# Performance work log

Measured on AMD Instinct MI355X. Metric: run time of the kernel, lower is better.

Reference implementation:

```python
import jax, jax.numpy as jnp
import numpy as np

N_NODES = 100000
N_EDGES = 1600000
K = 3  # TAGConv default hops


def _make_lin(key, out_dim, in_dim):
    # K+1 bias-free linears (stacked) + one shared output bias, per PyG TAGConv
    kw, = jax.random.split(key, 1)
    scale = 1.0 / np.sqrt(in_dim)
    W = jax.random.uniform(kw, (K + 1, out_dim, in_dim), jnp.float32, -scale, scale)
    b = jnp.zeros((out_dim,), jnp.float32)
    return W, b


def setup_inputs() -> dict:
    key = jax.random.key(0)
    ks = jax.random.split(key, 6)
    x = jax.random.normal(ks[0], (N_NODES, 128), jnp.float32)
    edge_index = jax.random.randint(ks[1], (2, N_EDGES), 0, N_NODES, jnp.int64)
    W1, b1 = _make_lin(ks[2], 128, 128)
    W2, b2 = _make_lin(ks[3], 64, 128)
    W3, b3 = _make_lin(ks[4], 16, 64)
    return {"x": x, "edge_index": edge_index, "W1": W1, "b1": b1,
            "W2": W2, "b2": b2, "W3": W3, "b3": b3}


def _tagconv(x, row, col, norm, W, b, n):
    # out = sum_k lin_k(A_norm^k x) + b ; message x_j*norm gathered at col
    out = jnp.einsum('nd,od->no', x, W[0])
    h = x
    for k in range(1, W.shape[0]):
        h = jax.ops.segment_sum(norm[:, None] * h[row], col, num_segments=n)
        out = out + jnp.einsum('nd,od->no', h, W[k])
    return out + b


def _dropout(x, key, p=0.5):
    keep = jax.random.bernoulli(key, 1.0 - p, x.shape)
    return jnp.where(keep, x / (1.0 - p), 0.0)


def reference(x, edge_index, W1, b1, W2, b2, W3, b3):
    n = x.shape[0]
    row, col = edge_index[0], edge_index[1]
    # gcn_norm without self-loops (TAGConv default)
    deg = jax.ops.segment_sum(jnp.ones(row.shape[0], x.dtype), col, num_segments=n)
    dis = jnp.where(deg > 0, 1.0 / jnp.sqrt(jnp.where(deg > 0, deg, 1.0)), 0.0)
    norm = dis[row] * dis[col]

    dk1, dk2 = jax.random.split(jax.random.key(42))
    h = _tagconv(x, row, col, norm, W1, b1, n)
    h = _dropout(h, dk1)
    h = _tagconv(h, row, col, norm, W2, b2, n)
    h = jax.nn.elu(h)
    h = _dropout(h, dk2)
    h = _tagconv(h, row, col, norm, W3, b3, n)
    return h
```

## Files before the change

kernel.cpp:

```cpp
#include <hip/hip_runtime.h>
#include <stdint.h>
#include <math.h>

#define N_NODES 100000
#define N_EDGES 1600000

typedef __bf16 bf16_t;
typedef __attribute__((ext_vector_type(4))) __bf16 bf16x4;
typedef __attribute__((ext_vector_type(8))) __bf16 bf16x8;
typedef __attribute__((ext_vector_type(4))) float f32x4;

__device__ __forceinline__ f32x4 mfma16(bf16x8 a, bf16x8 b, f32x4 c) {
  return __builtin_amdgcn_mfma_f32_16x16x32_bf16(a, b, c, 0, 0, 0);
}

__device__ __host__ __forceinline__ uint32_t rotl32(uint32_t v, int d) {
  return (v << d) | (v >> (32 - d));
}

__device__ __host__ __forceinline__ void threefry2x32(uint32_t k0, uint32_t k1,
                                                      uint32_t x0, uint32_t x1,
                                                      uint32_t& o0, uint32_t& o1) {
  uint32_t ks0 = k0, ks1 = k1, ks2 = k0 ^ k1 ^ 0x1BD11BDAu;
  x0 += ks0; x1 += ks1;
#define TF_R(r) { x0 += x1; x1 = rotl32(x1, r); x1 ^= x0; }
  TF_R(13) TF_R(15) TF_R(26) TF_R(6)
  x0 += ks1; x1 += ks2 + 1u;
  TF_R(17) TF_R(29) TF_R(16) TF_R(24)
  x0 += ks2; x1 += ks0 + 2u;
  TF_R(13) TF_R(15) TF_R(26) TF_R(6)
  x0 += ks0; x1 += ks1 + 3u;
  TF_R(17) TF_R(29) TF_R(16) TF_R(24)
  x0 += ks1; x1 += ks2 + 4u;
  TF_R(13) TF_R(15) TF_R(26) TF_R(6)
  x0 += ks2; x1 += ks0 + 5u;
#undef TF_R
  o0 = x0; o1 = x1;
}

__device__ __forceinline__ float drop_scale(uint32_t idx, uint32_t k0, uint32_t k1) {
  uint32_t o0, o1;
  threefry2x32(k0, k1, 0u, idx, o0, o1);
  uint32_t bits = o0 ^ o1;
  float u = __uint_as_float((bits >> 9) | 0x3f800000u) - 1.0f;
  return (u < 0.5f) ? 2.0f : 0.0f;
}

__global__ __launch_bounds__(256) void detect_kernel(const int* __restrict__ ei,
                                                     int* __restrict__ found_nonzero) {
  int idx = blockIdx.x * 256 + threadIdx.x;
  size_t j = (size_t)idx * 781;
  if (ei[2 * j + 1] != 0) atomicOr(found_nonzero, 1);
}

__device__ __forceinline__ int edge_row(const int* ei, bool i32, int e) {
  return i32 ? ei[e] : ei[2 * (size_t)e];
}
__device__ __forceinline__ int edge_col(const int* ei, bool i32, int e) {
  return i32 ? ei[N_EDGES + e] : ei[2 * ((size_t)N_EDGES + (size_t)e)];
}

#define BKT_SHIFT 8
#define NBKT 391
#define BKT_CAP 6144
#define EPB 8192
#define NBLK 196
#define SCAN_M (NBKT * NBLK)

__global__ __launch_bounds__(256) void hist_kernel(const int* __restrict__ ei,
                                                   const int* __restrict__ flag,
                                                   int* __restrict__ hist) {
  __shared__ int h[NBKT];
  const int t = threadIdx.x, blk = blockIdx.x;
  for (int i = t; i < NBKT; i += 256) h[i] = 0;
  __syncthreads();
  const bool i32 = *flag != 0;
  const int e0 = blk * EPB;
  for (int i = t; i < EPB; i += 256) {
    int e = e0 + i;
    if (e < N_EDGES) atomicAdd(&h[edge_col(ei, i32, e) >> BKT_SHIFT], 1);
  }
  __syncthreads();
  for (int i = t; i < NBKT; i += 256) hist[i * NBLK + blk] = h[i];
}

__global__ __launch_bounds__(1024) void binscan_kernel(const int* __restrict__ hist,
                                                       int* __restrict__ S) {
  __shared__ int sh[1024];
  const int t = threadIdx.x;
  const int CH = (SCAN_M + 1023) / 1024;
  int lo = t * CH, hi = min(lo + CH, SCAN_M);
  int s = 0;
  for (int i = lo; i < hi; ++i) s += hist[i];
  sh[t] = s;
  __syncthreads();
  for (int ofs = 1; ofs < 1024; ofs <<= 1) {
    int u = (t >= ofs) ? sh[t - ofs] : 0;
    __syncthreads();
    sh[t] += u;
    __syncthreads();
  }
  int p = sh[t] - s;
  for (int i = lo; i < hi; ++i) { S[i] = p; p += hist[i]; }
  if (t == 1023) S[SCAN_M] = p;
}

__global__ __launch_bounds__(256) void binfill_kernel(const int* __restrict__ ei,
                                                      const int* __restrict__ flag,
                                                      const int* __restrict__ S,
                                                      int2* __restrict__ bins) {
  __shared__ int cur[NBKT];
  const int t = threadIdx.x, blk = blockIdx.x;
  for (int i = t; i < NBKT; i += 256) cur[i] = S[i * NBLK + blk];
  __syncthreads();
  const bool i32 = *flag != 0;
  const int e0 = blk * EPB;
  for (int i = t; i < EPB; i += 256) {
    int e = e0 + i;
    if (e < N_EDGES) {
      int r = edge_row(ei, i32, e);
      int c = edge_col(ei, i32, e);
      int p = atomicAdd(&cur[c >> BKT_SHIFT], 1);
      bins[p] = make_int2(r, c);
    }
  }
}

__global__ __launch_bounds__(512) void degdis_kernel(const int2* __restrict__ bins,
                                                     const int* __restrict__ S,
                                                     float* __restrict__ dis,
                                                     int* __restrict__ rptr) {
  __shared__ int h[256];
  __shared__ int sc[256];
  const int b = blockIdx.x, t = threadIdx.x;
  const int Bb = S[b * NBLK];
  const int Be = S[(b + 1) * NBLK];
  if (t < 256) h[t] = 0;
  __syncthreads();
  for (int i = t; i < Be - Bb; i += 512)
    atomicAdd(&h[bins[Bb + i].y & 255], 1);
  __syncthreads();
  if (t < 256) sc[t] = h[t];
  __syncthreads();
  for (int ofs = 1; ofs < 256; ofs <<= 1) {
    int u = 0;
    if (t >= ofs && t < 256) u = sc[t - ofs];
    __syncthreads();
    if (t < 256) sc[t] += u;
    __syncthreads();
  }
  const int c0 = b << BKT_SHIFT;
  if (t < 256 && c0 + t < N_NODES) {
    int d = h[t];
    dis[c0 + t] = (d > 0) ? (1.0f / sqrtf((float)d)) : 0.0f;
    rptr[c0 + t] = Bb + sc[t] - d;
  }
  if (b == NBKT - 1 && t == 0) rptr[N_NODES] = N_EDGES;
}

__global__ __launch_bounds__(512) void scatter_kernel(
    const int2* __restrict__ bins, const float* __restrict__ dis,
    const int* __restrict__ rptr, int2* __restrict__ erec) {
  __shared__ int loff[256];
  __shared__ int lcur[256];
  __shared__ float ldis[256];
  __shared__ int2 stage[BKT_CAP];
  const int b = blockIdx.x;
  const int c0 = b << BKT_SHIFT;
  const int nn = min(256, N_NODES - c0);
  const int t = threadIdx.x;
  const int base = rptr[c0];
  if (t < nn) {
    loff[t] = rptr[c0 + t] - base;
    lcur[t] = 0;
    ldis[t] = dis[c0 + t];
  }
  __syncthreads();
  const int cnt = min(rptr[c0 + nn] - base, BKT_CAP);
  for (int i = t; i < cnt; i += 512) {
    int2 rec = bins[base + i];
    int lc = rec.y & 255;
    float nrm = dis[rec.x] * ldis[lc];
    int p = atomicAdd(&lcur[lc], 1);
    stage[loff[lc] + p] = make_int2(rec.x, __float_as_int(nrm));
  }
  __syncthreads();
  for (int i = t; i < cnt; i += 512) erec[base + i] = stage[i];
}

__global__ __launch_bounds__(256) void wcvt_kernel(
    const float* __restrict__ W1, const float* __restrict__ W2,
    const float* __restrict__ W3,
    bf16_t* __restrict__ Wb1, bf16_t* __restrict__ Wb2,
    bf16_t* __restrict__ Wb3) {
  int i = blockIdx.x * 256 + threadIdx.x;
  if (i < 65536) Wb1[i] = (bf16_t)W1[i];
  if (i < 32768) Wb2[i] = (bf16_t)W2[i];
  if (i < 4096)  Wb3[i] = (bf16_t)W3[i];
}

template <int DIN, int LOG_DOUT, int NCH, bool YB, bool AHL>
__global__ __launch_bounds__(256) void matmul_mfma_kernel(
    const void* __restrict__ hA, const void* __restrict__ hAlo,
    const bf16_t* __restrict__ Wb, const float* __restrict__ bias,
    float* __restrict__ y0, void* __restrict__ y1,
    void* __restrict__ y2, void* __restrict__ y3) {
  constexpr int LDK = DIN + 8;
  constexpr int DOUT = 1 << LOG_DOUT;
  constexpr int KI = DIN / 32;
  __shared__ bf16_t sm[2][64 * LDK];
  const int m0 = blockIdx.x * 64;
  const int tid = threadIdx.x;

  if (AHL) {
    constexpr int NL = 64 * DIN / 8 / 256;
#pragma unroll
    for (int it = 0; it < NL; ++it) {
      int idx = tid + it * 256;
      int r = idx / (DIN / 8), cc = (idx % (DIN / 8)) * 8;
      int gm = m0 + r;
      uint4 vh = make_uint4(0, 0, 0, 0), vl = make_uint4(0, 0, 0, 0);
      if (gm < N_NODES) {
        vh = ((const uint4*)hA)[((size_t)gm * DIN + cc) >> 3];
        vl = ((const uint4*)hAlo)[((size_t)gm * DIN + cc) >> 3];
      }
      *(uint4*)&sm[0][r * LDK + cc] = vh;
      *(uint4*)&sm[1][r * LDK + cc] = vl;
    }
  } else {
    constexpr int NL = 64 * DIN / 4 / 256;
    union U4 { bf16_t b[4]; uint2 u; };
#pragma unroll
    for (int it = 0; it < NL; ++it) {
      int idx = tid + it * 256;
      int r = idx / (DIN / 4), cc = (idx % (DIN / 4)) * 4;
      int gm = m0 + r;
      float4 v = (gm < N_NODES) ? ((const float4*)hA)[((size_t)gm * DIN + cc) >> 2]
                                : make_float4(0.f, 0.f, 0.f, 0.f);
      U4 hi, lo;
      hi.b[0] = (bf16_t)v.x; lo.b[0] = (bf16_t)(v.x - (float)hi.b[0]);
      hi.b[1] = (bf16_t)v.y; lo.b[1] = (bf16_t)(v.y - (float)hi.b[1]);
      hi.b[2] = (bf16_t)v.z; lo.b[2] = (bf16_t)(v.z - (float)hi.b[2]);
      hi.b[3] = (bf16_t)v.w; lo.b[3] = (bf16_t)(v.w - (float)hi.b[3]);
      *(uint2*)&sm[0][r * LDK + cc] = hi.u;
      *(uint2*)&sm[1][r * LDK + cc] = lo.u;
    }
  }
  __syncthreads();

  const int w = tid >> 6, lane = tid & 63;
  const int wm = w & 1, wn = w >> 1;
  const int quad = lane >> 4, lr = lane & 15;

  bf16x8 aH[2][KI], aL[2][KI];
#pragma unroll
  for (int mt = 0; mt < 2; ++mt)
#pragma unroll
    for (int ki = 0; ki < KI; ++ki) {
      int rowa = wm * 32 + mt * 16 + lr;
      int koff = ki * 32 + quad * 8;
      aH[mt][ki] = *(const bf16x8*)&sm[0][rowa * LDK + koff];
      aL[mt][ki] = *(const bf16x8*)&sm[1][rowa * LDK + koff];
    }
  __syncthreads();

  constexpr int NLB = 64 * DIN / 8 / 256;
  uint4 wreg[NLB];
#pragma unroll
  for (int it = 0; it < NLB; ++it) {
    int idx = tid + it * 256;
    int r = idx / (DIN / 8), cc = (idx % (DIN / 8)) * 8;
    wreg[it] = ((const uint4*)Wb)[(((size_t)r) * DIN + cc) >> 3];
    *(uint4*)&sm[0][r * LDK + cc] = wreg[it];
  }
  __syncthreads();

  for (int nc = 0; nc < NCH; ++nc) {
    int p = nc & 1;
    if (nc + 1 < NCH) {
#pragma unroll
      for (int it = 0; it < NLB; ++it) {
        int idx = tid + it * 256;
        int r = idx / (DIN / 8), cc = (idx % (DIN / 8)) * 8;
        wreg[it] = ((const uint4*)Wb)[(((size_t)((nc + 1) * 64 + r)) * DIN + cc) >> 3];
      }
    }

    f32x4 acc[2][2] = {};
#pragma unroll
    for (int ki = 0; ki < KI; ++ki) {
      int koff = ki * 32 + quad * 8;
      bf16x8 bfr[2];
#pragma unroll
      for (int nt = 0; nt < 2; ++nt)
        bfr[nt] = *(const bf16x8*)&sm[p][(wn * 32 + nt * 16 + lr) * LDK + koff];
#pragma unroll
      for (int mt = 0; mt < 2; ++mt)
#pragma unroll
        for (int nt = 0; nt < 2; ++nt) {
          acc[mt][nt] = mfma16(bfr[nt], aH[mt][ki], acc[mt][nt]);
          acc[mt][nt] = mfma16(bfr[nt], aL[mt][ki], acc[mt][nt]);
        }
    }

    if (nc + 1 < NCH) {
#pragma unroll
      for (int it = 0; it < NLB; ++it) {
        int idx = tid + it * 256;
        int r = idx / (DIN / 8), cc = (idx % (DIN / 8)) * 8;
        *(uint4*)&sm[p ^ 1][r * LDK + cc] = wreg[it];
      }
    }
    __syncthreads();

    const int n0 = nc * 64;
#pragma unroll
    for (int mt = 0; mt < 2; ++mt) {
      int m = m0 + wm * 32 + mt * 16 + lr;
      if (m >= N_NODES) continue;
#pragma unroll
      for (int nt = 0; nt < 2; ++nt) {
        int nb = n0 + wn * 32 + nt * 16 + quad * 4;
        int k = nb >> LOG_DOUT;
        int o = nb & (DOUT - 1);
        size_t oi = (size_t)m * DOUT + o;
        if (k == 0) {
          float4 bv = *(const float4*)&bias[o];
          float4 st = make_float4(acc[mt][nt][0] + bv.x, acc[mt][nt][1] + bv.y,
                                  acc[mt][nt][2] + bv.z, acc[mt][nt][3] + bv.w);
          *(float4*)&y0[oi] = st;
        } else {
          void* yk = (k == 1) ? y1 : (k == 2) ? y2 : y3;
          if (YB) {
            bf16x4 bb;
            bb.x = (bf16_t)acc[mt][nt][0];
            bb.y = (bf16_t)acc[mt][nt][1];
            bb.z = (bf16_t)acc[mt][nt][2];
            bb.w = (bf16_t)acc[mt][nt][3];
            *(bf16x4*)((bf16_t*)yk + oi) = bb;
          } else {
            *(f32x4*)((float*)yk + oi) = acc[mt][nt];
          }
        }
      }
    }
  }
}

template <int D, int EPI, bool ZBF, bool ABF, int OMODE>
__global__ __launch_bounds__(256) void prop_kernel(
    const void* __restrict__ zv, const void* __restrict__ addv,
    void* __restrict__ outv, void* __restrict__ outv2,
    const int* __restrict__ rptr, const int2* __restrict__ erec,
    uint32_t k0, uint32_t k1) {
  constexpr int LPN = D / 4;
  constexpr int NPB = 256 / LPN;
  int lane = threadIdx.x % LPN;
  int nsub = threadIdx.x / LPN;
  int c = blockIdx.x * NPB + nsub;
  if (c >= N_NODES) return;
  int e0 = rptr[c], e1 = rptr[c + 1];
  float a0 = 0.f, a1 = 0.f, a2 = 0.f, a3 = 0.f;

  auto ld = [&](int r, float v[4]) {
    if (ZBF) {
      bf16x4 t = ((const bf16x4*)zv)[(size_t)r * LPN + lane];
      v[0] = (float)t.x; v[1] = (float)t.y; v[2] = (float)t.z; v[3] = (float)t.w;
    } else {
      float4 t = ((const float4*)zv)[(size_t)r * LPN + lane];
      v[0] = t.x; v[1] = t.y; v[2] = t.z; v[3] = t.w;
    }
  };

  int e = e0;
  for (; e + 3 < e1; e += 4) {
    int2 q[4];
    float v[4][4];
#pragma unroll
    for (int j = 0; j < 4; ++j) q[j] = erec[e + j];
#pragma unroll
    for (int j = 0; j < 4; ++j) ld(q[j].x, v[j]);
#pragma unroll
    for (int j = 0; j < 4; ++j) {
      float wv = __int_as_float(q[j].y);
      a0 = fmaf(wv, v[j][0], a0);
      a1 = fmaf(wv, v[j][1], a1);
      a2 = fmaf(wv, v[j][2], a2);
      a3 = fmaf(wv, v[j][3], a3);
    }
  }
  for (; e < e1; ++e) {
    int2 q = erec[e];
    float wv = __int_as_float(q.y);
    float v[4];
    ld(q.x, v);
    a0 = fmaf(wv, v[0], a0);
    a1 = fmaf(wv, v[1], a1);
    a2 = fmaf(wv, v[2], a2);
    a3 = fmaf(wv, v[3], a3);
  }

  size_t pidx = (size_t)c * LPN + lane;
  uint32_t fidx = (uint32_t)c * D + 4 * lane;
  float ax[4];
  if (ABF) {
    bf16x4 t = ((const bf16x4*)addv)[pidx];
    ax[0] = (float)t.x; ax[1] = (float)t.y; ax[2] = (float)t.z; ax[3] = (float)t.w;
  } else {
    float4 t = ((const float4*)addv)[pidx];
    ax[0] = t.x; ax[1] = t.y; ax[2] = t.z; ax[3] = t.w;
  }
  float o[4] = {a0 + ax[0], a1 + ax[1], a2 + ax[2], a3 + ax[3]};
  if (EPI == 1) {
#pragma unroll
    for (int j = 0; j < 4; ++j) o[j] *= drop_scale(fidx + j, k0, k1);
  }
  if (EPI == 2) {
#pragma unroll
    for (int j = 0; j < 4; ++j) {
      o[j] = (o[j] > 0.f) ? o[j] : expm1f(o[j]);
      o[j] *= drop_scale(fidx + j, k0, k1);
    }
  }
  if (OMODE == 0) {
    ((float4*)outv)[pidx] = make_float4(o[0], o[1], o[2], o[3]);
  } else if (OMODE == 1) {
    bf16x4 bv;
    bv.x = (bf16_t)o[0]; bv.y = (bf16_t)o[1];
    bv.z = (bf16_t)o[2]; bv.w = (bf16_t)o[3];
    ((bf16x4*)outv)[pidx] = bv;
  } else {
    bf16x4 hv, lv;
    hv.x = (bf16_t)o[0]; hv.y = (bf16_t)o[1];
    hv.z = (bf16_t)o[2]; hv.w = (bf16_t)o[3];
    lv.x = (bf16_t)(o[0] - (float)hv.x);
    lv.y = (bf16_t)(o[1] - (float)hv.y);
    lv.z = (bf16_t)(o[2] - (float)hv.z);
    lv.w = (bf16_t)(o[3] - (float)hv.w);
    ((bf16x4*)outv)[pidx] = hv;
    ((bf16x4*)outv2)[pidx] = lv;
  }
}

extern "C" void kernel_launch(void* const* d_in, const int* in_sizes, int n_in,
                              void* d_out, int out_size, void* d_ws, size_t ws_size,
                              hipStream_t stream) {
  const float* x  = (const float*)d_in[0];
  const int*   ei = (const int*)d_in[1];
  const float* W1 = (const float*)d_in[2];
  const float* b1 = (const float*)d_in[3];
  const float* W2 = (const float*)d_in[4];
  const float* b2 = (const float*)d_in[5];
  const float* W3 = (const float*)d_in[6];
  const float* b3 = (const float*)d_in[7];
  float* out = (float*)d_out;

  char* ws = (char*)d_ws;
  size_t off = 0;
  auto alloc = [&](size_t bytes) -> char* {
    char* p = ws + off;
    off += (bytes + 255) & ~(size_t)255;
    return p;
  };
  int*   flag   = (int*)alloc(256);
  float* dis    = (float*)alloc((size_t)N_NODES * 4);
  int*   rptr   = (int*)alloc((size_t)(N_NODES + 1) * 4);
  int*   hist   = (int*)alloc((size_t)SCAN_M * 4);
  int*   S      = (int*)alloc((size_t)(SCAN_M + 1) * 4);
  int2*  erec   = (int2*)alloc((size_t)N_EDGES * 8);
  bf16_t* Wb1  = (bf16_t*)alloc(65536 * 2);
  bf16_t* Wb2  = (bf16_t*)alloc(32768 * 2);
  bf16_t* Wb3  = (bf16_t*)alloc(4096 * 2);
  float*  R0  = (float*)alloc((size_t)N_NODES * 128 * 4);
  float*  R2  = (float*)alloc((size_t)N_NODES * 16 * 4);
  bf16_t* Zb0 = (bf16_t*)alloc((size_t)N_NODES * 128 * 2);
  bf16_t* Zb1 = (bf16_t*)alloc((size_t)N_NODES * 128 * 2);
  bf16_t* Bb1 = (bf16_t*)alloc((size_t)N_NODES * 128 * 2);
  bf16_t* Bb2 = (bf16_t*)alloc((size_t)N_NODES * 128 * 2);

  int2* bins = (int2*)R0;

  hipMemsetAsync(flag, 0, 256, stream);

  detect_kernel<<<8, 256, 0, stream>>>(ei, flag);
  hist_kernel<<<NBLK, 256, 0, stream>>>(ei, flag, hist);
  binscan_kernel<<<1, 1024, 0, stream>>>(hist, S);
  binfill_kernel<<<NBLK, 256, 0, stream>>>(ei, flag, S, bins);
  degdis_kernel<<<NBKT, 512, 0, stream>>>(bins, S, dis, rptr);
  scatter_kernel<<<NBKT, 512, 0, stream>>>(bins, dis, rptr, erec);
  wcvt_kernel<<<256, 256, 0, stream>>>(W1, W2, W3, Wb1, Wb2, Wb3);

  uint32_t d10, d11, d20, d21;
  threefry2x32(0u, 42u, 0u, 0u, d10, d11);
  threefry2x32(0u, 42u, 0u, 1u, d20, d21);

  const int MB = (N_NODES + 63) / 64;
  const int PB128 = (N_NODES + 7) / 8;
  const int PB64n = (N_NODES + 15) / 16;
  const int PB16n = (N_NODES + 63) / 64;

  matmul_mfma_kernel<128, 7, 8, true, false><<<MB, 256, 0, stream>>>(
      x, nullptr, Wb1, b1, R0, Bb1, Bb2, Zb0);
  prop_kernel<128, 0, true, true, 1><<<PB128, 256, 0, stream>>>(
      Zb0, Bb2, Zb1, nullptr, rptr, erec, 0, 0);
  prop_kernel<128, 0, true, true, 1><<<PB128, 256, 0, stream>>>(
      Zb1, Bb1, Zb0, nullptr, rptr, erec, 0, 0);
  prop_kernel<128, 1, true, false, 2><<<PB128, 256, 0, stream>>>(
      Zb0, R0, Bb2, Bb1, rptr, erec, d10, d11);

  float*  R1f = R0;
  bf16_t* S0 = Zb0;
  bf16_t* S1 = Zb0 + (size_t)N_NODES * 64;
  bf16_t* S2 = Zb1;
  bf16_t* S3 = Zb1 + (size_t)N_NODES * 64;
  matmul_mfma_kernel<128, 6, 4, true, true><<<MB, 256, 0, stream>>>(
      Bb2, Bb1, Wb2, b2, R1f, S2, S3, S0);
  prop_kernel<64, 0, true, true, 1><<<PB64n, 256, 0, stream>>>(
      S0, S3, S1, nullptr, rptr, erec, 0, 0);
  prop_kernel<64, 0, true, true, 1><<<PB64n, 256, 0, stream>>>(
      S1, S2, S0, nullptr, rptr, erec, 0, 0);
  prop_kernel<64, 2, true, false, 2><<<PB64n, 256, 0, stream>>>(
      S0, R1f, S2, S3, rptr, erec, d20, d21);

  float*  z0f = R2;
  bf16_t* zb1 = Bb1;
  bf16_t* zb2 = Bb1 + (size_t)N_NODES * 16;
  bf16_t* zb3 = Bb1 + (size_t)N_NODES * 32;
  matmul_mfma_kernel<64, 4, 1, true, true><<<MB, 256, 0, stream>>>(
      S2, S3, Wb3, b3, z0f, zb1, zb2, zb3);
  prop_kernel<16, 0, true, true, 1><<<PB16n, 256, 0, stream>>>(
      zb3, zb2, zb2, nullptr, rptr, erec, 0, 0);
  prop_kernel<16, 0, true, true, 1><<<PB16n, 256, 0, stream>>>(
      zb2, zb1, zb1, nullptr, rptr, erec, 0, 0);
  prop_kernel<16, 0, true, false, 0><<<PB16n, 256, 0, stream>>>(
      zb1, z0f, out, nullptr, rptr, erec, 0, 0);

  (void)in_sizes; (void)n_in; (void)out_size; (void)ws_size;
}
```

Before: 768.1 us.

## Replace single-block histogram scan with three-stage multi-block scan

The global exclusive scan over the bucket-by-block histogram ran in one 1024-thread block, with each thread serially walking a chunk. It is now split into a per-bucket reduction, a single-block scan of the bucket totals, and a per-bucket in-block scan that adds the bucket base. This spreads the scan across many CUs to cut the serial latency, at the cost of two extra kernel launches. The bscan2 kernel assumes NBLK is at most 256 and bbase assumes NBKT is at most 512.

```diff
diff --git a/kernel.cpp b/kernel.cpp
--- a/kernel.cpp
+++ b/kernel.cpp
@@ -84,25 +84,54 @@
   for (int i = t; i < NBKT; i += 256) hist[i * NBLK + blk] = h[i];
 }
 
-__global__ __launch_bounds__(1024) void binscan_kernel(const int* __restrict__ hist,
-                                                       int* __restrict__ S) {
-  __shared__ int sh[1024];
+__global__ __launch_bounds__(256) void btot_kernel(const int* __restrict__ hist,
+                                                   int* __restrict__ btot) {
+  __shared__ int sh[256];
+  const int b = blockIdx.x, t = threadIdx.x;
+  int s = 0;
+  for (int i = t; i < NBLK; i += 256) s += hist[b * NBLK + i];
+  sh[t] = s;
+  __syncthreads();
+  for (int ofs = 128; ofs > 0; ofs >>= 1) {
+    if (t < ofs) sh[t] += sh[t + ofs];
+    __syncthreads();
+  }
+  if (t == 0) btot[b] = sh[0];
+}
+
+__global__ __launch_bounds__(512) void bbase_kernel(const int* __restrict__ btot,
+                                                    int* __restrict__ bbase,
+                                                    int* __restrict__ S) {
+  __shared__ int sh[512];
   const int t = threadIdx.x;
-  const int CH = (SCAN_M + 1023) / 1024;
-  int lo = t * CH, hi = min(lo + CH, SCAN_M);
-  int s = 0;
-  for (int i = lo; i < hi; ++i) s += hist[i];
-  sh[t] = s;
-  __syncthreads();
-  for (int ofs = 1; ofs < 1024; ofs <<= 1) {
+  int v = (t < NBKT) ? btot[t] : 0;
+  sh[t] = v;
+  __syncthreads();
+  for (int ofs = 1; ofs < 512; ofs <<= 1) {
     int u = (t >= ofs) ? sh[t - ofs] : 0;
     __syncthreads();
     sh[t] += u;
     __syncthreads();
   }
-  int p = sh[t] - s;
-  for (int i = lo; i < hi; ++i) { S[i] = p; p += hist[i]; }
-  if (t == 1023) S[SCAN_M] = p;
+  if (t < NBKT) bbase[t] = sh[t] - v;
+  if (t == 0) S[SCAN_M] = N_EDGES;
+}
+
+__global__ __launch_bounds__(256) void bscan2_kernel(const int* __restrict__ hist,
+                                                     const int* __restrict__ bbase,
+                                                     int* __restrict__ S) {
+  __shared__ int sh[256];
+  const int b = blockIdx.x, t = threadIdx.x;
+  int v = (t < NBLK) ? hist[b * NBLK + t] : 0;
+  sh[t] = v;
+  __syncthreads();
+  for (int ofs = 1; ofs < 256; ofs <<= 1) {
+    int u = (t >= ofs) ? sh[t - ofs] : 0;
+    __syncthreads();
+    sh[t] += u;
+    __syncthreads();
+  }
+  if (t < NBLK) S[b * NBLK + t] = bbase[b] + sh[t] - v;
 }
 
 __global__ __launch_bounds__(256) void binfill_kernel(const int* __restrict__ ei,
@@ -467,6 +496,8 @@
   int*   rptr   = (int*)alloc((size_t)(N_NODES + 1) * 4);
   int*   hist   = (int*)alloc((size_t)SCAN_M * 4);
   int*   S      = (int*)alloc((size_t)(SCAN_M + 1) * 4);
+  int*   btot   = (int*)alloc((size_t)NBKT * 4);
+  int*   bbase  = (int*)alloc((size_t)NBKT * 4);
   int2*  erec   = (int2*)alloc((size_t)N_EDGES * 8);
   bf16_t* Wb1  = (bf16_t*)alloc(65536 * 2);
   bf16_t* Wb2  = (bf16_t*)alloc(32768 * 2);
@@ -484,7 +515,9 @@
 
   detect_kernel<<<8, 256, 0, stream>>>(ei, flag);
   hist_kernel<<<NBLK, 256, 0, stream>>>(ei, flag, hist);
-  binscan_kernel<<<1, 1024, 0, stream>>>(hist, S);
+  btot_kernel<<<NBKT, 256, 0, stream>>>(hist, btot);
+  bbase_kernel<<<1, 512, 0, stream>>>(btot, bbase, S);
+  bscan2_kernel<<<NBKT, 256, 0, stream>>>(hist, bbase, S);
   binfill_kernel<<<NBLK, 256, 0, stream>>>(ei, flag, S, bins);
   degdis_kernel<<<NBKT, 512, 0, stream>>>(bins, S, dis, rptr);
   scatter_kernel<<<NBKT, 512, 0, stream>>>(bins, dis, rptr, erec);
```

After: 656.8 us. 1.17x faster.
